# Kernel tuning notes

Measured on AMD Instinct MI355X. Metric: run time of the kernel, lower is better.

## Reference

```python
import jax, jax.numpy as jnp
import numpy as np

N, E, B = 100000, 400000, 4096      # nodes, directed edges, graphs
P, d = 4, 49                        # phm_dim, per-component dim; D = P*d = 196
L = 3                               # message-passing layers
D1, D2 = 64, 32                     # downstream per-component dims (256/4, 128/4)


def setup_inputs():
    key = jax.random.key(0)
    ks = jax.random.split(key, 20)
    def nrm(k, shape, s=0.1):
        return jax.random.normal(k, shape, dtype=jnp.float32) * s
    return {
        "x": jax.random.randint(ks[0], (N, 9), 0, 119),
        "edge_index": jax.random.randint(ks[1], (2, E), 0, N),
        "edge_attr": jax.random.randint(ks[2], (E, 3), 0, 8),
        "batch": jnp.sort(jax.random.randint(ks[3], (N,), 0, B)),
        # encoders: summed categorical embeddings in hypercomplex form [*, P, d]
        "atom_emb": nrm(ks[4], (9, 119, P, d)),
        "bond_emb": nrm(ks[5], (L, 3, 8, P, d)),
        # per-layer PHM conv: contribution matrices A (phm rule) + component weights W
        "conv_A": nrm(ks[6], (L, P, P, P), 0.5),
        "conv_W": nrm(ks[7], (L, P, d, d)),
        "conv_b": jnp.zeros((L, P, d), jnp.float32),
        "mp_gamma": jnp.ones((L, P * d), jnp.float32),
        "mp_beta": jnp.zeros((L, P * d), jnp.float32),
        # soft-attention pooling: PHM linear + real transformer gate
        "pool_A": nrm(ks[8], (P, P, P), 0.5),
        "pool_W": nrm(ks[9], (P, d, d)),
        "pool_b": jnp.zeros((P, d), jnp.float32),
        "pool_rt_w": nrm(ks[10], (P,), 0.5),
        "pool_rt_b": jnp.zeros((d,), jnp.float32),
        # downstream PHM MLP 196 -> 256 -> 128 -> 4*1, then real trafo -> 1
        "dn_A": nrm(ks[11], (3, P, P, P), 0.5),
        "dn1_W": nrm(ks[12], (P, d, D1)),
        "dn1_b": jnp.zeros((P, D1), jnp.float32),
        "dn1_gamma": jnp.ones((P * D1,), jnp.float32),
        "dn1_beta": jnp.zeros((P * D1,), jnp.float32),
        "dn2_W": nrm(ks[13], (P, D1, D2)),
        "dn2_b": jnp.zeros((P, D2), jnp.float32),
        "dn2_gamma": jnp.ones((P * D2,), jnp.float32),
        "dn2_beta": jnp.zeros((P * D2,), jnp.float32),
        "dn3_W": nrm(ks[14], (P, D2, 1)),
        "dn3_b": jnp.zeros((P, 1), jnp.float32),
        "rt_w": nrm(ks[15], (P,), 0.5),
        "rt_b": jnp.zeros((1,), jnp.float32),
    }


def phm_linear(x, A, W, b):
    # PHM linear: y = x @ (sum_i kron(A_i, W_i)) + b, on [n, P, din] -> [n, P, dout]
    return jnp.einsum('nkp,ikj,ipq->njq', x, A, W) + b


def naive_bn(x, gamma, beta, eps=1e-5):
    # naive batch norm over the batch axis, per flattened hypercomplex feature
    n, p, dd = x.shape
    x2 = x.reshape(n, p * dd)
    mu = x2.mean(axis=0)
    var = x2.var(axis=0)
    x2 = (x2 - mu) * jax.lax.rsqrt(var + eps) * gamma + beta
    return x2.reshape(n, p, dd)


def reference(x, edge_index, edge_attr, batch, atom_emb, bond_emb,
              conv_A, conv_W, conv_b, mp_gamma, mp_beta,
              pool_A, pool_W, pool_b, pool_rt_w, pool_rt_b,
              dn_A, dn1_W, dn1_b, dn1_gamma, dn1_beta,
              dn2_W, dn2_b, dn2_gamma, dn2_beta, dn3_W, dn3_b, rt_w, rt_b):
    src, dst = edge_index[0], edge_index[1]
    # atom encoder: sum embeddings of 9 categorical features -> [N, P, d]
    h0 = atom_emb[jnp.arange(9), x].sum(axis=1)
    h = h0
    for l in range(L):  # small fixed layer count
        # bond encoder for this layer -> [E, P, d]
        e = bond_emb[l][jnp.arange(3), edge_attr].sum(axis=1)
        # message = x_j + e_ij (identity msg encoder); self-loop (zero edge feat) adds h
        m = h[src] + e
        agg = jax.ops.segment_sum(m, dst, num_segments=N) + h
        z = phm_linear(agg, conv_A[l], conv_W[l], conv_b[l])
        z = jax.nn.relu(naive_bn(z, mp_gamma[l], mp_beta[l]))
        h = z + h0  # skip-connect to first embedding (sc_type='first')
    # soft-attention pooling: real-valued sigmoid gate per node feature
    g = jax.nn.sigmoid(
        jnp.einsum('npk,p->nk', phm_linear(h, pool_A, pool_W, pool_b), pool_rt_w)
        + pool_rt_b)
    pooled = jax.ops.segment_sum(h * g[:, None, :], batch, num_segments=B)  # [B, P, d]
    # downstream PHM MLP with naive batch norm + relu
    z = jax.nn.relu(naive_bn(phm_linear(pooled, dn_A[0], dn1_W, dn1_b), dn1_gamma, dn1_beta))
    z = jax.nn.relu(naive_bn(phm_linear(z, dn_A[1], dn2_W, dn2_b), dn2_gamma, dn2_beta))
    o = phm_linear(z, dn_A[2], dn3_W, dn3_b)          # [B, P, 1]
    return jnp.einsum('npk,p->nk', o, rt_w) + rt_b    # [B, 1]
```

## Files before the change

### kernel.cpp

```cpp
#include <hip/hip_runtime.h>
#include <cstdint>
#include <cstddef>

#define N_NODES 100000
#define N_EDGES 400000
#define N_GRAPHS 4096
#define DF 196
#define DD 49
#define NPB 5
#define TST 200
#define WSLOT2 7168
#define ESTF 116

#define AS1 __attribute__((address_space(1)))
#define AS3 __attribute__((address_space(3)))

typedef __bf16 bf16x8 __attribute__((ext_vector_type(8)));
typedef float f32x4 __attribute__((ext_vector_type(4)));

__device__ __forceinline__ unsigned short f2bf(float f) {
  unsigned int u = __float_as_uint(f);
  u = u + 0x7FFFu + ((u >> 16) & 1u);
  return (unsigned short)(u >> 16);
}
__device__ __forceinline__ float bf2f(unsigned short h) {
  return __uint_as_float(((unsigned int)h) << 16);
}

__global__ void convert_wfrag_kernel(const float* __restrict__ cA,
                                     const float* __restrict__ cW,
                                     unsigned short* __restrict__ wfrag) {
  int idx = blockIdx.x * blockDim.x + threadIdx.x;
  if (idx >= 3 * 100352) return;
  int l = idx / 100352;
  int r = idx - l * 100352;
  int ct = r / 7168; int r1 = r - ct * 7168;
  int ks = r1 / 1024; int r2 = r1 - ks * 1024;
  int h = r2 / 512;  int r3 = r2 - h * 512;
  int ln = r3 / 8;   int j = r3 - ln * 8;
  int col = ct * 16 + (ln & 15);
  int k = ks * 32 + (ln >> 4) * 8 + j;
  float v = 0.f;
  if (col < DF && k < DF) {
    int k4 = k / DD, p = k - (k / DD) * DD;
    int j4 = col / DD, q = col - (col / DD) * DD;
#pragma unroll
    for (int i = 0; i < 4; i++)
      v += cA[((l * 4 + i) * 4 + k4) * 4 + j4] * cW[((l * 4 + i) * DD + p) * DD + q];
  }
  unsigned short hi = f2bf(v);
  wfrag[idx] = (h == 0) ? hi : f2bf(v - bf2f(hi));
}

__global__ void setup_small_kernel(const float* __restrict__ bond, float* __restrict__ lut,
                                   const float* __restrict__ pA, const float* __restrict__ pW,
                                   const float* __restrict__ pb, const float* __restrict__ rtw,
                                   const float* __restrict__ rtb,
                                   unsigned short* __restrict__ wfragG,
                                   float* __restrict__ gbias,
                                   const float* __restrict__ dnA,
                                   const float* __restrict__ W1, const float* __restrict__ W2,
                                   const float* __restrict__ W3,
                                   float* __restrict__ M1, float* __restrict__ M2,
                                   float* __restrict__ M3) {
  int idx0 = blockIdx.x * blockDim.x + threadIdx.x;
  const int NL = 3 * 512 * DF;
  const int NGF = 28672;
  const int NB2 = 64;
  const int n1 = DF * 256, n2 = 256 * 128, n3 = 128 * 4;
  if (idx0 < NL) {
    int idx = idx0;
    int l = idx / (512 * DF);
    int r = idx - l * (512 * DF);
    int code = r / DF, c = r - (r / DF) * DF;
    int a0 = code & 7, a1 = (code >> 3) & 7, a2 = (code >> 6) & 7;
    lut[idx] = bond[((l * 3 + 0) * 8 + a0) * DF + c]
             + bond[((l * 3 + 1) * 8 + a1) * DF + c]
             + bond[((l * 3 + 2) * 8 + a2) * DF + c];
  } else if (idx0 < NL + NGF) {
    int idx = idx0 - NL;
    int ct = idx / 7168; int r1 = idx - ct * 7168;
    int ks = r1 / 1024; int r2 = r1 - ks * 1024;
    int h = r2 / 512;  int r3 = r2 - h * 512;
    int ln = r3 / 8;   int j = r3 - ln * 8;
    int col = ct * 16 + (ln & 15);
    int k = ks * 32 + (ln >> 4) * 8 + j;
    float v = 0.f;
    if (col < DD && k < DF) {
      int kp = k / DD, p = k - (k / DD) * DD;
#pragma unroll
      for (int i = 0; i < 4; i++) {
        float aw = 0.f;
#pragma unroll
        for (int j4 = 0; j4 < 4; j4++) aw += pA[(i * 4 + kp) * 4 + j4] * rtw[j4];
        v += aw * pW[(i * DD + p) * DD + col];
      }
    }
    unsigned short hi = f2bf(v);
    wfragG[idx] = (h == 0) ? hi : f2bf(v - bf2f(hi));
  } else if (idx0 < NL + NGF + NB2) {
    int q = idx0 - NL - NGF;
    if (q < DD) {
      float s = rtb[q];
#pragma unroll
      for (int j = 0; j < 4; j++) s += rtw[j] * pb[j * DD + q];
      gbias[q] = s;
    }
  } else if (idx0 < NL + NGF + NB2 + n1 + n2 + n3) {
    int idx = idx0 - NL - NGF - NB2;
    if (idx < n1) {
      int r = idx >> 8, c = idx & 255;
      int k = r / DD, p = r - (r / DD) * DD;
      int j = c >> 6, Q = c & 63;
      float s = 0.f;
#pragma unroll
      for (int i = 0; i < 4; i++) s += dnA[i * 16 + k * 4 + j] * W1[(i * DD + p) * 64 + Q];
      M1[idx] = s;
    } else if (idx < n1 + n2) {
      int m = idx - n1;
      int r = m >> 7, c = m & 127;
      int k = r >> 6, p = r & 63, j = c >> 5, q = c & 31;
      float s = 0.f;
#pragma unroll
      for (int i = 0; i < 4; i++) s += dnA[64 + i * 16 + k * 4 + j] * W2[(i * 64 + p) * 32 + q];
      M2[m] = s;
    } else {
      int m = idx - n1 - n2;
      int r = m >> 2, j = m & 3;
      int k = r >> 5, p = r & 31;
      float s = 0.f;
#pragma unroll
      for (int i = 0; i < 4; i++) s += dnA[128 + i * 16 + k * 4 + j] * W3[i * 32 + p];
      M3[m] = s;
    }
  }
}

__global__ void hist_kernel(const int* __restrict__ dst, int* __restrict__ counts) {
  int e = blockIdx.x * blockDim.x + threadIdx.x;
  if (e < N_EDGES) atomicAdd(&counts[dst[e]], 1);
}

__global__ void scan_local_kernel(const int* __restrict__ counts, int* __restrict__ offs,
                                  int* __restrict__ bsum) {
  __shared__ int sm[256];
  int tid = threadIdx.x;
  int gid = blockIdx.x * 256 + tid;
  int v = (gid < N_NODES) ? counts[gid] : 0;
  sm[tid] = v;
  __syncthreads();
  for (int d = 1; d < 256; d <<= 1) {
    int add = (tid >= d) ? sm[tid - d] : 0;
    __syncthreads();
    sm[tid] += add;
    __syncthreads();
  }
  if (gid < N_NODES) offs[gid] = sm[tid] - v;
  if (tid == 255) bsum[blockIdx.x] = sm[255];
}

__global__ void scan_bsum_kernel(int* __restrict__ bsum, int* __restrict__ bpre, int nb) {
  __shared__ int sm[512];
  int tid = threadIdx.x;
  int v = (tid < nb) ? bsum[tid] : 0;
  sm[tid] = v;
  __syncthreads();
  for (int d = 1; d < 512; d <<= 1) {
    int add = (tid >= d) ? sm[tid - d] : 0;
    __syncthreads();
    sm[tid] += add;
    __syncthreads();
  }
  if (tid < nb) bpre[tid] = sm[tid] - v;
}

__global__ void add_off_kernel(int* __restrict__ offs, const int* __restrict__ bpre) {
  int gid = blockIdx.x * blockDim.x + threadIdx.x;
  if (gid < N_NODES) offs[gid] += bpre[gid >> 8];
  if (gid == 0) offs[N_NODES] = N_EDGES;
}

__global__ void scatter_kernel(const int* __restrict__ src, const int* __restrict__ dst,
                               const int* __restrict__ ea, int* __restrict__ counts,
                               const int* __restrict__ offs,
                               unsigned int* __restrict__ sorted) {
  int e = blockIdx.x * blockDim.x + threadIdx.x;
  if (e >= N_EDGES) return;
  int d = dst[e];
  int code = ea[e * 3 + 0] | (ea[e * 3 + 1] << 3) | (ea[e * 3 + 2] << 6);
  int pos = offs[d] + atomicSub(&counts[d], 1) - 1;
  sorted[pos] = (unsigned int)src[e] | ((unsigned int)code << 17);
}

__global__ void sortseg_kernel(const int* __restrict__ offs,
                               unsigned int* __restrict__ sorted) {
  int n = blockIdx.x * blockDim.x + threadIdx.x;
  if (n >= N_NODES) return;
  int s = offs[n], e = offs[n + 1];
  for (int i = s + 1; i < e; i++) {
    unsigned int v = sorted[i];
    int j = i - 1;
    while (j >= s && sorted[j] > v) { sorted[j + 1] = sorted[j]; j--; }
    sorted[j + 1] = v;
  }
}

__global__ void atom_enc_kernel(const int* __restrict__ x, const float* __restrict__ emb,
                                float* __restrict__ h0) {
  int idx = blockIdx.x * blockDim.x + threadIdx.x;
  if (idx >= N_NODES * DF) return;
  int n = idx / DF;
  int c = idx - n * DF;
  float s = 0.f;
#pragma unroll
  for (int f = 0; f < 9; f++) {
    int xi = x[n * 9 + f];
    s += emb[(f * 119 + xi) * DF + c];
  }
  h0[idx] = s;
}

__global__ __launch_bounds__(256)
void agg_kernel(const float* __restrict__ h, const int* __restrict__ offs,
                const unsigned int* __restrict__ sorted, const float* __restrict__ lut,
                unsigned short* __restrict__ tH, unsigned short* __restrict__ tL) {
  int t = threadIdx.x;
  int i = t / 49, q = t - i * 49;
  if (i >= NPB) return;
  int node = blockIdx.x * NPB + i;
  if (node >= N_NODES) return;
  const float4* h4 = (const float4*)h;
  const float4* l4 = (const float4*)lut;
  float4 acc = h4[(size_t)node * 49 + q];
  int s = offs[node], e = offs[node + 1];
  int k = s;
  for (; k + 2 <= e; k += 2) {
    unsigned int se0 = sorted[k];
    unsigned int se1 = sorted[k + 1];
    int s0 = se0 & 0x1FFFF, c0 = se0 >> 17;
    int s1 = se1 & 0x1FFFF, c1 = se1 >> 17;
    float4 hv0 = h4[(size_t)s0 * 49 + q];
    float4 lv0 = l4[(size_t)c0 * 49 + q];
    float4 hv1 = h4[(size_t)s1 * 49 + q];
    float4 lv1 = l4[(size_t)c1 * 49 + q];
    acc.x += (hv0.x + lv0.x) + (hv1.x + lv1.x);
    acc.y += (hv0.y + lv0.y) + (hv1.y + lv1.y);
    acc.z += (hv0.z + lv0.z) + (hv1.z + lv1.z);
    acc.w += (hv0.w + lv0.w) + (hv1.w + lv1.w);
  }
  if (k < e) {
    unsigned int se = sorted[k];
    int srcn = se & 0x1FFFF;
    int code = se >> 17;
    float4 hv = h4[(size_t)srcn * 49 + q];
    float4 lv = l4[(size_t)code * 49 + q];
    acc.x += hv.x + lv.x;
    acc.y += hv.y + lv.y;
    acc.z += hv.z + lv.z;
    acc.w += hv.w + lv.w;
  }
  ushort4 hh, ll;
  hh.x = f2bf(acc.x); ll.x = f2bf(acc.x - bf2f(hh.x));
  hh.y = f2bf(acc.y); ll.y = f2bf(acc.y - bf2f(hh.y));
  hh.z = f2bf(acc.z); ll.z = f2bf(acc.z - bf2f(hh.z));
  hh.w = f2bf(acc.w); ll.w = f2bf(acc.w - bf2f(hh.w));
  size_t ob = (size_t)node * TST + q * 4;
  *(ushort4*)(tH + ob) = hh;
  *(ushort4*)(tL + ob) = ll;
  if (q == 48) {
    ushort4 z = make_ushort4(0, 0, 0, 0);
    *(ushort4*)(tH + (size_t)node * TST + 196) = z;
    *(ushort4*)(tL + (size_t)node * TST + 196) = z;
  }
}

__global__ __launch_bounds__(256, 2)
void conv_mfma_kernel(const unsigned short* __restrict__ tH,
                      const unsigned short* __restrict__ tL,
                      const unsigned short* __restrict__ wfrag,
                      const float* __restrict__ bias,
                      float* __restrict__ zout,
                      float* __restrict__ stats) {
  __shared__ __align__(16) unsigned short smW[14848];
  const int t = threadIdx.x;
  const int lane = t & 63;
  const int w = t >> 6;
  const int li = lane & 15;
  const int rg = lane >> 4;
  const int rb = blockIdx.x >> 1;
  const int ch = blockIdx.x & 1;
  const int rowbase = rb * 128 + w * 32;
  const unsigned short* wsrc = wfrag + (size_t)ch * 7 * 7168;

  f32x4 acc[2][7];
#pragma unroll
  for (int rt = 0; rt < 2; rt++)
#pragma unroll
    for (int ct = 0; ct < 7; ct++) acc[rt][ct] = (f32x4){0.f, 0.f, 0.f, 0.f};

  uint4 b0h[2], b0l[2], b1h[2], b1l[2], b2h[2], b2l[2], b3h[2], b3l[2];

#define LOADA(ks, aH, aL)                                                      \
  {                                                                            \
    _Pragma("unroll") for (int rt = 0; rt < 2; rt++) {                         \
      size_t o = (size_t)(rowbase + rt * 16 + li) * TST + (ks) * 32 + rg * 8;  \
      aH[rt] = *(const uint4*)(tH + o);                                        \
      aL[rt] = *(const uint4*)(tL + o);                                        \
    }                                                                          \
  }

#define WLOAD(ks, sbase)                                                       \
  {                                                                            \
    _Pragma("unroll") for (int f0 = 0; f0 < 4; f0++) {                         \
      int g = f0 * 4 + w;                                                      \
      if (g < 14) {                                                            \
        int hh = g & 1, ct = g >> 1;                                           \
        __builtin_amdgcn_global_load_lds(                                      \
            (AS1 const void*)(wsrc + ((size_t)(ct * 7 + (ks)) * 2 + hh) * 512 + lane * 8), \
            (AS3 void*)(smW + (sbase) + (ct * 2 + hh) * 512), 16, 0, 0);       \
      }                                                                        \
    }                                                                          \
  }

#define COMPUTE(sbase, aH, aL)                                                 \
  {                                                                            \
    _Pragma("unroll") for (int ct = 0; ct < 7; ct++) {                         \
      bf16x8 bh = *(const bf16x8*)(smW + (sbase) + ((ct * 2 + 0) * 512 + lane * 8)); \
      bf16x8 bl = *(const bf16x8*)(smW + (sbase) + ((ct * 2 + 1) * 512 + lane * 8)); \
      _Pragma("unroll") for (int rt = 0; rt < 2; rt++) {                       \
        bf16x8 ah = *(const bf16x8*)&aH[rt];                                   \
        bf16x8 al = *(const bf16x8*)&aL[rt];                                   \
        acc[rt][ct] = __builtin_amdgcn_mfma_f32_16x16x32_bf16(ah, bh, acc[rt][ct], 0, 0, 0); \
        acc[rt][ct] = __builtin_amdgcn_mfma_f32_16x16x32_bf16(al, bh, acc[rt][ct], 0, 0, 0); \
        acc[rt][ct] = __builtin_amdgcn_mfma_f32_16x16x32_bf16(ah, bl, acc[rt][ct], 0, 0, 0); \
      }                                                                        \
    }                                                                          \
  }

#define BARC(N)                                                                \
  {                                                                            \
    asm volatile("s_waitcnt vmcnt(" #N ")" ::: "memory");                      \
    __builtin_amdgcn_s_barrier();                                              \
  }
#define PINW() __builtin_amdgcn_sched_barrier(0)

  WLOAD(0, 0);
  PINW();
  LOADA(0, b0h, b0l);
  LOADA(1, b1h, b1l);
  LOADA(2, b2h, b2l);
  BARC(12);
  WLOAD(1, WSLOT2); PINW(); LOADA(3, b3h, b3l); COMPUTE(0, b0h, b0l);      BARC(4);
  WLOAD(2, 0);      PINW(); LOADA(4, b0h, b0l); COMPUTE(WSLOT2, b1h, b1l); BARC(4);
  WLOAD(3, WSLOT2); PINW(); LOADA(5, b1h, b1l); COMPUTE(0, b2h, b2l);      BARC(4);
  WLOAD(4, 0);      PINW(); LOADA(6, b2h, b2l); COMPUTE(WSLOT2, b3h, b3l); BARC(4);
  WLOAD(5, WSLOT2); PINW();                     COMPUTE(0, b0h, b0l);      BARC(0);
  WLOAD(6, 0);      PINW();                     COMPUTE(WSLOT2, b1h, b1l); BARC(0);
  COMPUTE(0, b2h, b2l);

  float part[7], psq[7];
#pragma unroll
  for (int ct = 0; ct < 7; ct++) { part[ct] = 0.f; psq[ct] = 0.f; }

  float* lz = (float*)smW;
  const int NU = ch ? 21 : 28;

#pragma unroll
  for (int half = 0; half < 2; half++) {
    __syncthreads();
    if ((w >> 1) == half) {
      int rl0 = (w & 1) * 32;
#pragma unroll
      for (int ct = 0; ct < 7; ct++) {
        int cl = ct * 16 + li;
        int cg = ch * 112 + cl;
        float bv = (cg < DF) ? bias[cg] : 0.f;
#pragma unroll
        for (int rt = 0; rt < 2; rt++) {
#pragma unroll
          for (int r = 0; r < 4; r++) {
            int row = rl0 + rt * 16 + rg * 4 + r;
            int gr = rowbase + rt * 16 + rg * 4 + r;
            float y = acc[rt][ct][r] + bv;
            if (gr < N_NODES && cg < DF) { part[ct] += y; psq[ct] += y * y; }
            lz[row * ESTF + cl] = y;
          }
        }
      }
    }
    __syncthreads();
    for (int idx = t; idx < 64 * NU; idx += 256) {
      int row = idx / NU, u = idx - (idx / NU) * NU;
      int gr = rb * 128 + half * 64 + row;
      if (gr < N_NODES) {
        float4 v = *(const float4*)(lz + row * ESTF + u * 4);
        *(float4*)(zout + (size_t)gr * DF + ch * 112 + u * 4) = v;
      }
    }
  }

  __syncthreads();
  float* redS = (float*)smW;
  float* redQ = redS + 4 * 112;
#pragma unroll
  for (int ct = 0; ct < 7; ct++) {
    float p = part[ct], q = psq[ct];
    p += __shfl_xor(p, 16, 64); p += __shfl_xor(p, 32, 64);
    q += __shfl_xor(q, 16, 64); q += __shfl_xor(q, 32, 64);
    if (rg == 0) { redS[w * 112 + ct * 16 + li] = p; redQ[w * 112 + ct * 16 + li] = q; }
  }
  __syncthreads();
  if (t < 112) {
    int cg = ch * 112 + t;
    if (cg < DF) {
      float s1 = redS[t] + redS[112 + t] + redS[224 + t] + redS[336 + t];
      float s2 = redQ[t] + redQ[112 + t] + redQ[224 + t] + redQ[336 + t];
      atomicAdd(&stats[cg], s1);
      atomicAdd(&stats[DF + cg], s2);
    }
  }
#undef LOADA
#undef WLOAD
#undef COMPUTE
#undef BARC
#undef PINW
}

__global__ void bn_relu_split_kernel(const float* __restrict__ stats,
                                     const float* __restrict__ gamma,
                                     const float* __restrict__ beta,
                                     const float* __restrict__ h0,
                                     float* __restrict__ h,
                                     unsigned short* __restrict__ tH,
                                     unsigned short* __restrict__ tL,
                                     int write_split) {
  int idx = blockIdx.x * blockDim.x + threadIdx.x;
  if (idx >= N_NODES * DD) return;
  int n = idx / DD, q = idx - (idx / DD) * DD;
  size_t fb = (size_t)n * DF + q * 4;
  float4 zv = *(const float4*)(h + fb);
  float4 sk = *(const float4*)(h0 + fb);
  int c = q * 4;
  const float invN = 1.f / N_NODES;
  float4 o;
  {
    float mu = stats[c + 0] * invN;
    float var = stats[DF + c + 0] * invN - mu * mu;
    o.x = fmaxf((zv.x - mu) * rsqrtf(var + 1e-5f) * gamma[c + 0] + beta[c + 0], 0.f) + sk.x;
  }
  {
    float mu = stats[c + 1] * invN;
    float var = stats[DF + c + 1] * invN - mu * mu;
    o.y = fmaxf((zv.y - mu) * rsqrtf(var + 1e-5f) * gamma[c + 1] + beta[c + 1], 0.f) + sk.y;
  }
  {
    float mu = stats[c + 2] * invN;
    float var = stats[DF + c + 2] * invN - mu * mu;
    o.z = fmaxf((zv.z - mu) * rsqrtf(var + 1e-5f) * gamma[c + 2] + beta[c + 2], 0.f) + sk.z;
  }
  {
    float mu = stats[c + 3] * invN;
    float var = stats[DF + c + 3] * invN - mu * mu;
    o.w = fmaxf((zv.w - mu) * rsqrtf(var + 1e-5f) * gamma[c + 3] + beta[c + 3], 0.f) + sk.w;
  }
  *(float4*)(h + fb) = o;
  if (write_split) {
    size_t ib = (size_t)n * TST + q * 4;
    ushort4 sh, sl;
    sh.x = f2bf(o.x); sl.x = f2bf(o.x - bf2f(sh.x));
    sh.y = f2bf(o.y); sl.y = f2bf(o.y - bf2f(sh.y));
    sh.z = f2bf(o.z); sl.z = f2bf(o.z - bf2f(sh.z));
    sh.w = f2bf(o.w); sl.w = f2bf(o.w - bf2f(sh.w));
    *(ushort4*)(tH + ib) = sh;
    *(ushort4*)(tL + ib) = sl;
  }
}

__global__ __launch_bounds__(256, 2)
void gate_mfma_kernel(const unsigned short* __restrict__ tH,
                      const unsigned short* __restrict__ tL,
                      const unsigned short* __restrict__ wfragG,
                      const float* __restrict__ gbias,
                      float* __restrict__ g) {
  __shared__ __align__(16) unsigned short smW[28672];
  const int t = threadIdx.x;
  const int lane = t & 63;
  const int w = t >> 6;
  const int li = lane & 15;
  const int rg = lane >> 4;
  const int rowbase = blockIdx.x * 128 + w * 32;

  f32x4 acc[2][4];
#pragma unroll
  for (int rt = 0; rt < 2; rt++)
#pragma unroll
    for (int ct = 0; ct < 4; ct++) acc[rt][ct] = (f32x4){0.f, 0.f, 0.f, 0.f};

  uint4 b0h[2], b0l[2], b1h[2], b1l[2], b2h[2], b2l[2], b3h[2], b3l[2];

#define LOADA(ks, aH, aL)                                                      \
  {                                                                            \
    _Pragma("unroll") for (int rt = 0; rt < 2; rt++) {                         \
      size_t o = (size_t)(rowbase + rt * 16 + li) * TST + (ks) * 32 + rg * 8;  \
      aH[rt] = *(const uint4*)(tH + o);                                        \
      aL[rt] = *(const uint4*)(tL + o);                                        \
    }                                                                          \
  }

#define COMPUTE(ks, aH, aL)                                                    \
  {                                                                            \
    _Pragma("unroll") for (int ct = 0; ct < 4; ct++) {                         \
      bf16x8 bh = *(const bf16x8*)(smW + ((ct * 7 + (ks)) * 2 + 0) * 512 + lane * 8); \
      bf16x8 bl = *(const bf16x8*)(smW + ((ct * 7 + (ks)) * 2 + 1) * 512 + lane * 8); \
      _Pragma("unroll") for (int rt = 0; rt < 2; rt++) {                       \
        bf16x8 ah = *(const bf16x8*)&aH[rt];                                   \
        bf16x8 al = *(const bf16x8*)&aL[rt];                                   \
        acc[rt][ct] = __builtin_amdgcn_mfma_f32_16x16x32_bf16(ah, bh, acc[rt][ct], 0, 0, 0); \
        acc[rt][ct] = __builtin_amdgcn_mfma_f32_16x16x32_bf16(al, bh, acc[rt][ct], 0, 0, 0); \
        acc[rt][ct] = __builtin_amdgcn_mfma_f32_16x16x32_bf16(ah, bl, acc[rt][ct], 0, 0, 0); \
      }                                                                        \
    }                                                                          \
  }

  LOADA(0, b0h, b0l);
  LOADA(1, b1h, b1l);
  LOADA(2, b2h, b2l);
  for (int i = t; i < 3584; i += 256)
    *(uint4*)(smW + (size_t)i * 8) = *(const uint4*)(wfragG + (size_t)i * 8);
  __syncthreads();
  LOADA(3, b3h, b3l); COMPUTE(0, b0h, b0l);
  LOADA(4, b0h, b0l); COMPUTE(1, b1h, b1l);
  LOADA(5, b1h, b1l); COMPUTE(2, b2h, b2l);
  LOADA(6, b2h, b2l); COMPUTE(3, b3h, b3l);
  COMPUTE(4, b0h, b0l);
  COMPUTE(5, b1h, b1l);
  COMPUTE(6, b2h, b2l);

#pragma unroll
  for (int ct = 0; ct < 4; ct++) {
    int c = ct * 16 + li;
    if (c < DD) {
      float bv = gbias[c];
#pragma unroll
      for (int rt = 0; rt < 2; rt++) {
#pragma unroll
        for (int r = 0; r < 4; r++) {
          int gr = rowbase + rt * 16 + rg * 4 + r;
          if (gr < N_NODES) {
            float v = acc[rt][ct][r] + bv;
            g[(size_t)gr * DD + c] = 1.f / (1.f + __expf(-v));
          }
        }
      }
    }
  }
#undef LOADA
#undef COMPUTE
}

template<int S, int MODE>
__launch_bounds__(256)
__global__ void gemm_kernel(const float* X, const float* __restrict__ W,
                            const float* __restrict__ bias, float* Y,
                            float* __restrict__ stats, int Nrows, int K, int NC) {
  constexpr int WN = S * 64;
  __shared__ __align__(16) float At[32][64];
  __shared__ __align__(16) float Wl[32][WN];
  const int t = threadIdx.x;
  const int tx = t & 15;
  const int ty = t >> 4;
  const int r0 = blockIdx.x * 64;

  float acc[S][4][4];
#pragma unroll
  for (int s = 0; s < S; s++)
#pragma unroll
    for (int i = 0; i < 4; i++)
#pragma unroll
      for (int j = 0; j < 4; j++) acc[s][i][j] = 0.f;

  const int lr = t >> 2;
  const int kb = (t & 3) * 8;
  constexpr int TPR = S * 16;
  const int cw = (t % TPR) * 4;
  const int kr = t / TPR;
  constexpr int RPP = 256 / TPR;
  constexpr int PASSES = 32 / RPP;

  for (int k0 = 0; k0 < K; k0 += 32) {
    {
      const int gr = r0 + lr;
      const float* xp = X + (size_t)gr * K + k0 + kb;
      if (gr < Nrows && (k0 + kb + 7) < K) {
        float4 v0 = *(const float4*)(xp);
        float4 v1 = *(const float4*)(xp + 4);
        At[kb + 0][lr] = v0.x; At[kb + 1][lr] = v0.y;
        At[kb + 2][lr] = v0.z; At[kb + 3][lr] = v0.w;
        At[kb + 4][lr] = v1.x; At[kb + 5][lr] = v1.y;
        At[kb + 6][lr] = v1.z; At[kb + 7][lr] = v1.w;
      } else {
#pragma unroll
        for (int i = 0; i < 8; i++) {
          int kk = kb + i;
          float v = 0.f;
          if (gr < Nrows && (k0 + kk) < K) v = xp[i];
          At[kk][lr] = v;
        }
      }
    }
#pragma unroll
    for (int ps = 0; ps < PASSES; ps++) {
      int kk = kr + ps * RPP;
      int gk = k0 + kk;
      if (gk < K && (cw + 3) < NC && ((NC & 3) == 0)) {
        float4 v = *(const float4*)(W + (size_t)gk * NC + cw);
        Wl[kk][cw + 0] = v.x; Wl[kk][cw + 1] = v.y;
        Wl[kk][cw + 2] = v.z; Wl[kk][cw + 3] = v.w;
      } else {
#pragma unroll
        for (int j = 0; j < 4; j++) {
          int c = cw + j;
          float v = 0.f;
          if (gk < K && c < NC) v = W[(size_t)gk * NC + c];
          Wl[kk][c] = v;
        }
      }
    }
    __syncthreads();
#pragma unroll 4
    for (int kk = 0; kk < 32; kk++) {
      float4 a = *(const float4*)&At[kk][ty * 4];
      float av[4] = {a.x, a.y, a.z, a.w};
#pragma unroll
      for (int s = 0; s < S; s++) {
        float4 w = *(const float4*)&Wl[kk][s * 64 + tx * 4];
        float wv[4] = {w.x, w.y, w.z, w.w};
#pragma unroll
        for (int i = 0; i < 4; i++)
#pragma unroll
          for (int j = 0; j < 4; j++)
            acc[s][i][j] = fmaf(av[i], wv[j], acc[s][i][j]);
      }
    }
    __syncthreads();
  }

#pragma unroll
  for (int s = 0; s < S; s++)
#pragma unroll
    for (int j = 0; j < 4; j++) {
      int c = s * 64 + tx * 4 + j;
      float bv = (c < NC) ? bias[c] : 0.f;
#pragma unroll
      for (int i = 0; i < 4; i++) {
        float y = acc[s][i][j] + bv;
        if (MODE == 1) y = 1.f / (1.f + __expf(-y));
        acc[s][i][j] = y;
      }
    }
#pragma unroll
  for (int i = 0; i < 4; i++) {
    int gr = r0 + ty * 4 + i;
    if (gr < Nrows) {
#pragma unroll
      for (int s = 0; s < S; s++)
#pragma unroll
        for (int j = 0; j < 4; j++) {
          int c = s * 64 + tx * 4 + j;
          if (c < NC) Y[(size_t)gr * NC + c] = acc[s][i][j];
        }
    }
  }
  if (MODE == 0) {
    float* red = &Wl[0][0];
    __syncthreads();
#pragma unroll
    for (int s = 0; s < S; s++)
#pragma unroll
      for (int j = 0; j < 4; j++) {
        float p = 0.f;
#pragma unroll
        for (int i = 0; i < 4; i++)
          if ((r0 + ty * 4 + i) < Nrows) p += acc[s][i][j];
        red[ty * WN + s * 64 + tx * 4 + j] = p;
      }
    __syncthreads();
    if (t < WN) {
      float tot = 0.f;
#pragma unroll
      for (int yy = 0; yy < 16; yy++) tot += red[yy * WN + t];
      if (t < NC) atomicAdd(&stats[t], tot);
    }
    __syncthreads();
#pragma unroll
    for (int s = 0; s < S; s++)
#pragma unroll
      for (int j = 0; j < 4; j++) {
        float p = 0.f;
#pragma unroll
        for (int i = 0; i < 4; i++)
          if ((r0 + ty * 4 + i) < Nrows) p += acc[s][i][j] * acc[s][i][j];
        red[ty * WN + s * 64 + tx * 4 + j] = p;
      }
    __syncthreads();
    if (t < WN) {
      float tot = 0.f;
#pragma unroll
      for (int yy = 0; yy < 16; yy++) tot += red[yy * WN + t];
      if (t < NC) atomicAdd(&stats[NC + t], tot);
    }
  }
}

__global__ void bn_relu_kernel(const float* __restrict__ z, const float* __restrict__ stats,
                               const float* __restrict__ gamma, const float* __restrict__ beta,
                               float* __restrict__ out,
                               int total, int NC, float invN) {
  int idx = blockIdx.x * blockDim.x + threadIdx.x;
  if (idx >= total) return;
  int c = idx % NC;
  float mu = stats[c] * invN;
  float var = stats[NC + c] * invN - mu * mu;
  float v = (z[idx] - mu) * rsqrtf(var + 1e-5f) * gamma[c] + beta[c];
  out[idx] = fmaxf(v, 0.f);
}

__device__ __forceinline__ int lower_bound_dev(const int* a, int n, int v) {
  int lo = 0, hi = n;
  while (lo < hi) { int mid = (lo + hi) >> 1; if (a[mid] < v) lo = mid + 1; else hi = mid; }
  return lo;
}

__global__ void pool_kernel(const float* __restrict__ h, const float* __restrict__ g,
                            const int* __restrict__ batch, float* __restrict__ pooled) {
  int b = blockIdx.x;
  __shared__ int bounds[2];
  if (threadIdx.x == 0) {
    bounds[0] = lower_bound_dev(batch, N_NODES, b);
    bounds[1] = lower_bound_dev(batch, N_NODES, b + 1);
  }
  __syncthreads();
  int c = threadIdx.x;
  if (c >= DF) return;
  int s = bounds[0], e = bounds[1];
  int q = c % DD;
  float acc = 0.f;
  for (int n = s; n < e; n++)
    acc = fmaf(h[(size_t)n * DF + c], g[(size_t)n * DD + q], acc);
  pooled[(size_t)b * DF + c] = acc;
}

__global__ void final_kernel(const float* __restrict__ z2, const float* __restrict__ M3,
                             const float* __restrict__ b3, const float* __restrict__ rtw,
                             const float* __restrict__ rtb, float* __restrict__ out) {
  __shared__ float sM[128 * 4];
  __shared__ float srw[4];
  __shared__ float srb;
  int t = threadIdx.x;
  for (int i = t; i < 512; i += 256) sM[i] = M3[i];
  if (t < 4) srw[t] = rtw[t];
  if (t == 4) srb = rtb[0];
  __syncthreads();
  int b = blockIdx.x * blockDim.x + t;
  if (b >= N_GRAPHS) return;
  float o0 = b3[0], o1 = b3[1], o2 = b3[2], o3 = b3[3];
  const float* zp = z2 + (size_t)b * 128;
  for (int p = 0; p < 128; p++) {
    float v = zp[p];
    o0 = fmaf(v, sM[p * 4 + 0], o0);
    o1 = fmaf(v, sM[p * 4 + 1], o1);
    o2 = fmaf(v, sM[p * 4 + 2], o2);
    o3 = fmaf(v, sM[p * 4 + 3], o3);
  }
  out[b] = srb + o0 * srw[0] + o1 * srw[1] + o2 * srw[2] + o3 * srw[3];
}

extern "C" void kernel_launch(void* const* d_in, const int* in_sizes, int n_in,
                              void* d_out, int out_size, void* d_ws, size_t ws_size,
                              hipStream_t stream) {
  (void)in_sizes; (void)n_in; (void)out_size; (void)ws_size;
  const int* x          = (const int*)d_in[0];
  const int* edge_index = (const int*)d_in[1];
  const int* edge_attr  = (const int*)d_in[2];
  const int* batch      = (const int*)d_in[3];
  const float* atom_emb = (const float*)d_in[4];
  const float* bond_emb = (const float*)d_in[5];
  const float* conv_A   = (const float*)d_in[6];
  const float* conv_W   = (const float*)d_in[7];
  const float* conv_b   = (const float*)d_in[8];
  const float* mp_gamma = (const float*)d_in[9];
  const float* mp_beta  = (const float*)d_in[10];
  const float* pool_A   = (const float*)d_in[11];
  const float* pool_W   = (const float*)d_in[12];
  const float* pool_b   = (const float*)d_in[13];
  const float* pool_rt_w = (const float*)d_in[14];
  const float* pool_rt_b = (const float*)d_in[15];
  const float* dn_A     = (const float*)d_in[16];
  const float* dn1_W    = (const float*)d_in[17];
  const float* dn1_b    = (const float*)d_in[18];
  const float* dn1_gamma = (const float*)d_in[19];
  const float* dn1_beta = (const float*)d_in[20];
  const float* dn2_W    = (const float*)d_in[21];
  const float* dn2_b    = (const float*)d_in[22];
  const float* dn2_gamma = (const float*)d_in[23];
  const float* dn2_beta = (const float*)d_in[24];
  const float* dn3_W    = (const float*)d_in[25];
  const float* dn3_b    = (const float*)d_in[26];
  const float* rt_w     = (const float*)d_in[27];
  const float* rt_b     = (const float*)d_in[28];
  float* out = (float*)d_out;

  char* ws = (char*)d_ws;
  size_t off = 0;
  auto alloc = [&](size_t bytes) -> char* {
    char* p = ws + off;
    off = (off + bytes + 255) & ~(size_t)255;
    return p;
  };
  const size_t HBYTES = (size_t)N_NODES * DF * sizeof(float);
  float* h0 = (float*)alloc(HBYTES);
  float* h  = (float*)alloc(HBYTES);
  unsigned short* tH = (unsigned short*)alloc((size_t)N_NODES * TST * 2 + 4096);
  unsigned short* tL = (unsigned short*)alloc((size_t)N_NODES * TST * 2 + 4096);
  float* g      = (float*)h0;
  float* pooled = (float*)((char*)h0 + (((size_t)N_NODES * DD * 4 + 255) & ~(size_t)255));
  float* z1     = (float*)((char*)pooled + (((size_t)N_GRAPHS * DF * 4 + 255) & ~(size_t)255));
  float* z2     = (float*)((char*)z1 + (((size_t)N_GRAPHS * 256 * 4 + 255) & ~(size_t)255));
  unsigned short* wfrag = (unsigned short*)alloc((size_t)3 * 100352 * 2);
  unsigned short* wfragG = (unsigned short*)alloc((size_t)28672 * 2);
  float* gbias  = (float*)alloc(64 * 4);
  float* M1     = (float*)alloc(DF * 256 * 4);
  float* M2     = (float*)alloc(256 * 128 * 4);
  float* M3     = (float*)alloc(128 * 4 * 4);
  float* stats  = (float*)alloc(2048 * 4);
  int*  counts  = (int*)alloc(N_NODES * 4);
  int*  offs    = (int*)alloc((N_NODES + 1) * 4);
  unsigned int* sorted = (unsigned int*)alloc((size_t)N_EDGES * 4);
  float* lut    = (float*)alloc((size_t)3 * 512 * DF * 4);
  int*  bsum    = (int*)alloc(512 * 4);
  int*  bpre    = (int*)alloc(512 * 4);

  const int* src = edge_index;
  const int* dst = edge_index + N_EDGES;
  const int NB = (N_NODES + 255) / 256;

  hipMemsetAsync(stats, 0, 2048 * 4, stream);
  hipMemsetAsync(counts, 0, N_NODES * 4, stream);

  convert_wfrag_kernel<<<(3 * 100352 + 255) / 256, 256, 0, stream>>>(conv_A, conv_W, wfrag);
  {
    const int total = 3 * 512 * DF + 28672 + 64 + (DF * 256 + 256 * 128 + 128 * 4);
    setup_small_kernel<<<(total + 255) / 256, 256, 0, stream>>>(
        bond_emb, lut, pool_A, pool_W, pool_b, pool_rt_w, pool_rt_b, wfragG, gbias,
        dn_A, dn1_W, dn2_W, dn3_W, M1, M2, M3);
  }

  hist_kernel<<<(N_EDGES + 255) / 256, 256, 0, stream>>>(dst, counts);
  scan_local_kernel<<<NB, 256, 0, stream>>>(counts, offs, bsum);
  scan_bsum_kernel<<<1, 512, 0, stream>>>(bsum, bpre, NB);
  add_off_kernel<<<NB, 256, 0, stream>>>(offs, bpre);
  scatter_kernel<<<(N_EDGES + 255) / 256, 256, 0, stream>>>(
      src, dst, edge_attr, counts, offs, sorted);
  sortseg_kernel<<<NB, 256, 0, stream>>>(offs, sorted);

  atom_enc_kernel<<<(N_NODES * DF + 255) / 256, 256, 0, stream>>>(x, atom_emb, h0);

  const int NROW = (N_NODES + 127) / 128;
  const int NCONV = NROW * 2;
  for (int l = 0; l < 3; l++) {
    const float* hl = (l == 0) ? h0 : h;
    agg_kernel<<<(N_NODES + NPB - 1) / NPB, 256, 0, stream>>>(
        hl, offs, sorted, lut + (size_t)l * 512 * DF, tH, tL);
    float* st = stats + l * 392;
    conv_mfma_kernel<<<NCONV, 256, 0, stream>>>(
        tH, tL, wfrag + (size_t)l * 100352, conv_b + (size_t)l * DF, h, st);
    bn_relu_split_kernel<<<(N_NODES * DD + 255) / 256, 256, 0, stream>>>(
        st, mp_gamma + l * DF, mp_beta + l * DF, h0, h, tH, tL, (l == 2) ? 1 : 0);
  }

  gate_mfma_kernel<<<NROW, 256, 0, stream>>>(tH, tL, wfragG, gbias, g);
  pool_kernel<<<N_GRAPHS, 256, 0, stream>>>(h, g, batch, pooled);

  gemm_kernel<4, 0><<<(N_GRAPHS + 63) / 64, 256, 0, stream>>>(
      pooled, M1, dn1_b, z1, stats + 1176, N_GRAPHS, DF, 256);
  bn_relu_kernel<<<(N_GRAPHS * 256 + 255) / 256, 256, 0, stream>>>(
      z1, stats + 1176, dn1_gamma, dn1_beta, z1, N_GRAPHS * 256, 256, 1.f / N_GRAPHS);
  gemm_kernel<2, 0><<<(N_GRAPHS + 63) / 64, 256, 0, stream>>>(
      z1, M2, dn2_b, z2, stats + 1688, N_GRAPHS, 256, 128);
  bn_relu_kernel<<<(N_GRAPHS * 128 + 255) / 256, 256, 0, stream>>>(
      z2, stats + 1688, dn2_gamma, dn2_beta, z2, N_GRAPHS * 128, 128, 1.f / N_GRAPHS);
  final_kernel<<<(N_GRAPHS + 255) / 256, 256, 0, stream>>>(z2, M3, dn3_b, rt_w, rt_b, out);
}
```

Measured before the change: 851.2 us.

## Single-buffer conv weight LDS to halve shared memory footprint

Replaces the double-buffered LDS weight slots in the conv MFMA kernel with a single slot, adding an LDS-read barrier before each weight refill. The epilogue staging is split into four 32-row passes so it fits in the smaller buffer. LDS per block drops from about 29 KB to about 14.5 KB, which could allow more resident blocks. The cost is that weight loads no longer overlap with compute, and the epilogue needs extra barriers.

```diff
diff --git a/kernel.cpp b/kernel.cpp
--- a/kernel.cpp
+++ b/kernel.cpp
@@ -9,7 +9,6 @@
 #define DD 49
 #define NPB 5
 #define TST 200
-#define WSLOT2 7168
 #define ESTF 116
 
 #define AS1 __attribute__((address_space(1)))
@@ -281,7 +280,7 @@
                       const float* __restrict__ bias,
                       float* __restrict__ zout,
                       float* __restrict__ stats) {
-  __shared__ __align__(16) unsigned short smW[14848];
+  __shared__ __align__(16) unsigned short smW[7424];
   const int t = threadIdx.x;
   const int lane = t & 63;
   const int w = t >> 6;
@@ -309,7 +308,7 @@
     }                                                                          \
   }
 
-#define WLOAD(ks, sbase)                                                       \
+#define WLOAD(ks)                                                              \
   {                                                                            \
     _Pragma("unroll") for (int f0 = 0; f0 < 4; f0++) {                         \
       int g = f0 * 4 + w;                                                      \
@@ -317,16 +316,16 @@
         int hh = g & 1, ct = g >> 1;                                           \
         __builtin_amdgcn_global_load_lds(                                      \
             (AS1 const void*)(wsrc + ((size_t)(ct * 7 + (ks)) * 2 + hh) * 512 + lane * 8), \
-            (AS3 void*)(smW + (sbase) + (ct * 2 + hh) * 512), 16, 0, 0);       \
+            (AS3 void*)(smW + (ct * 2 + hh) * 512), 16, 0, 0);                 \
       }                                                                        \
     }                                                                          \
   }
 
-#define COMPUTE(sbase, aH, aL)                                                 \
+#define COMPUTE(aH, aL)                                                        \
   {                                                                            \
     _Pragma("unroll") for (int ct = 0; ct < 7; ct++) {                         \
-      bf16x8 bh = *(const bf16x8*)(smW + (sbase) + ((ct * 2 + 0) * 512 + lane * 8)); \
-      bf16x8 bl = *(const bf16x8*)(smW + (sbase) + ((ct * 2 + 1) * 512 + lane * 8)); \
+      bf16x8 bh = *(const bf16x8*)(smW + ((ct * 2 + 0) * 512 + lane * 8));     \
+      bf16x8 bl = *(const bf16x8*)(smW + ((ct * 2 + 1) * 512 + lane * 8));     \
       _Pragma("unroll") for (int rt = 0; rt < 2; rt++) {                       \
         bf16x8 ah = *(const bf16x8*)&aH[rt];                                   \
         bf16x8 al = *(const bf16x8*)&aL[rt];                                   \
@@ -337,26 +336,43 @@
     }                                                                          \
   }
 
-#define BARC(N)                                                                \
+#define BARW(N)                                                                \
   {                                                                            \
     asm volatile("s_waitcnt vmcnt(" #N ")" ::: "memory");                      \
     __builtin_amdgcn_s_barrier();                                              \
   }
+#define BARL()                                                                 \
+  {                                                                            \
+    asm volatile("s_waitcnt lgkmcnt(0)" ::: "memory");                         \
+    __builtin_amdgcn_s_barrier();                                              \
+  }
 #define PINW() __builtin_amdgcn_sched_barrier(0)
 
-  WLOAD(0, 0);
+  WLOAD(0);
   PINW();
   LOADA(0, b0h, b0l);
   LOADA(1, b1h, b1l);
   LOADA(2, b2h, b2l);
-  BARC(12);
-  WLOAD(1, WSLOT2); PINW(); LOADA(3, b3h, b3l); COMPUTE(0, b0h, b0l);      BARC(4);
-  WLOAD(2, 0);      PINW(); LOADA(4, b0h, b0l); COMPUTE(WSLOT2, b1h, b1l); BARC(4);
-  WLOAD(3, WSLOT2); PINW(); LOADA(5, b1h, b1l); COMPUTE(0, b2h, b2l);      BARC(4);
-  WLOAD(4, 0);      PINW(); LOADA(6, b2h, b2l); COMPUTE(WSLOT2, b3h, b3l); BARC(4);
-  WLOAD(5, WSLOT2); PINW();                     COMPUTE(0, b0h, b0l);      BARC(0);
-  WLOAD(6, 0);      PINW();                     COMPUTE(WSLOT2, b1h, b1l); BARC(0);
-  COMPUTE(0, b2h, b2l);
+  BARW(12);
+  COMPUTE(b0h, b0l);
+  BARL();
+  WLOAD(1); PINW(); LOADA(3, b3h, b3l); BARW(4);
+  COMPUTE(b1h, b1l);
+  BARL();
+  WLOAD(2); PINW(); LOADA(4, b0h, b0l); BARW(4);
+  COMPUTE(b2h, b2l);
+  BARL();
+  WLOAD(3); PINW(); LOADA(5, b1h, b1l); BARW(4);
+  COMPUTE(b3h, b3l);
+  BARL();
+  WLOAD(4); PINW(); LOADA(6, b2h, b2l); BARW(4);
+  COMPUTE(b0h, b0l);
+  BARL();
+  WLOAD(5); PINW(); BARW(0);
+  COMPUTE(b1h, b1l);
+  BARL();
+  WLOAD(6); PINW(); BARW(0);
+  COMPUTE(b2h, b2l);
 
   float part[7], psq[7];
 #pragma unroll
@@ -366,10 +382,9 @@
   const int NU = ch ? 21 : 28;
 
 #pragma unroll
-  for (int half = 0; half < 2; half++) {
-    __syncthreads();
-    if ((w >> 1) == half) {
-      int rl0 = (w & 1) * 32;
+  for (int qt = 0; qt < 4; qt++) {
+    __syncthreads();
+    if (w == qt) {
 #pragma unroll
       for (int ct = 0; ct < 7; ct++) {
         int cl = ct * 16 + li;
@@ -379,7 +394,7 @@
         for (int rt = 0; rt < 2; rt++) {
 #pragma unroll
           for (int r = 0; r < 4; r++) {
-            int row = rl0 + rt * 16 + rg * 4 + r;
+            int row = rt * 16 + rg * 4 + r;
             int gr = rowbase + rt * 16 + rg * 4 + r;
             float y = acc[rt][ct][r] + bv;
             if (gr < N_NODES && cg < DF) { part[ct] += y; psq[ct] += y * y; }
@@ -389,9 +404,9 @@
       }
     }
     __syncthreads();
-    for (int idx = t; idx < 64 * NU; idx += 256) {
+    for (int idx = t; idx < 32 * NU; idx += 256) {
       int row = idx / NU, u = idx - (idx / NU) * NU;
-      int gr = rb * 128 + half * 64 + row;
+      int gr = rb * 128 + qt * 32 + row;
       if (gr < N_NODES) {
         float4 v = *(const float4*)(lz + row * ESTF + u * 4);
         *(float4*)(zout + (size_t)gr * DF + ch * 112 + u * 4) = v;
@@ -422,7 +437,8 @@
 #undef LOADA
 #undef WLOAD
 #undef COMPUTE
-#undef BARC
+#undef BARW
+#undef BARL
 #undef PINW
 }
 
```

Result: slower. 879.7 us (+3.4%).
